# Optimization experiments

Measured on AMD Instinct MI355X. Metric: run time of the kernel, lower is better.

The kernel has to match this reference:

```python
import jax, jax.numpy as jnp
import numpy as np

EPSILON = 1e-06

def setup_inputs() -> dict:
    key = jax.random.key(0)
    k1, k2, k3 = jax.random.split(key, 3)
    B, S, D = 4, 4096, 4096
    x = jax.random.normal(k1, (B, S, D), dtype=jnp.float32)
    residual = jax.random.normal(k2, (B, S, D), dtype=jnp.float32)
    gamma = jax.random.uniform(k3, (D,), dtype=jnp.float32)
    return {"x": x, "residual": residual, "gamma": gamma}

def reference(x, residual, gamma):
    # Pass 1: residual add + RMSNorm (row-wise over last dim)
    x_added = x + residual
    rstd = jax.lax.rsqrt(jnp.mean(jnp.square(x_added), axis=-1, keepdims=True) + EPSILON)
    output = x_added * rstd * gamma  # [B, S, D]
    # Pass 2: global abs-max dynamic int8 quantization
    max_val = jnp.max(jnp.abs(output))
    scale = max_val / 127.0
    q = jnp.clip(jnp.round(output / scale), -128, 127).astype(jnp.int8)
    return q
```

## Files before the change

kernel.cpp:

```cpp
#include <hip/hip_runtime.h>
#include <hip/hip_fp16.h>

#define DD 4096
#define NROWS 16384
#define EPS 1e-6f


struct H4 { __half2 a, b; };

__global__ __launch_bounds__(256) void pass1(
    const float* __restrict__ x, const float* __restrict__ res,
    const float* __restrict__ gamma, H4* __restrict__ yg,
    float* __restrict__ rstd, float* __restrict__ rowmax) {
  const int row = blockIdx.x;
  const int t = threadIdx.x;
  const float4* x4 = (const float4*)(x + (size_t)row * DD);
  const float4* r4 = (const float4*)(res + (size_t)row * DD);
  const float4* g4 = (const float4*)gamma;
  H4* yrow = yg + (size_t)row * (DD / 4);

  float ss = 0.f, mx = 0.f;
#pragma unroll
  for (int i = 0; i < 4; ++i) {
    const int idx = t + i * 256;
    float4 xv = x4[idx], rv = r4[idx], gv = g4[idx];
    float y0 = xv.x + rv.x, y1 = xv.y + rv.y;
    float y2 = xv.z + rv.z, y3 = xv.w + rv.w;
    ss += y0 * y0 + y1 * y1 + y2 * y2 + y3 * y3;
    float p0 = y0 * gv.x, p1 = y1 * gv.y, p2 = y2 * gv.z, p3 = y3 * gv.w;
    mx = fmaxf(mx, fmaxf(fmaxf(fabsf(p0), fabsf(p1)),
                         fmaxf(fabsf(p2), fabsf(p3))));
    H4 h;
    h.a = __floats2half2_rn(p0, p1);
    h.b = __floats2half2_rn(p2, p3);
    yrow[idx] = h;
  }

#pragma unroll
  for (int off = 32; off > 0; off >>= 1) {
    ss += __shfl_down(ss, off, 64);
    mx = fmaxf(mx, __shfl_down(mx, off, 64));
  }
  __shared__ float s_ss[4], s_mx[4];
  const int wave = t >> 6, lane = t & 63;
  if (lane == 0) { s_ss[wave] = ss; s_mx[wave] = mx; }
  __syncthreads();
  if (t == 0) {
    float tss = s_ss[0] + s_ss[1] + s_ss[2] + s_ss[3];
    float tmx = fmaxf(fmaxf(s_mx[0], s_mx[1]), fmaxf(s_mx[2], s_mx[3]));
    float rs = rsqrtf(tss * (1.0f / DD) + EPS);
    rstd[row] = rs;
    rowmax[row] = tmx * rs;
  }
}

__global__ __launch_bounds__(1024) void reduce_gmax(
    const float* __restrict__ rowmax, float* __restrict__ gmax) {
  const int t = threadIdx.x;
  float m = 0.f;
#pragma unroll
  for (int i = 0; i < NROWS / 1024; ++i) m = fmaxf(m, rowmax[t + i * 1024]);
#pragma unroll
  for (int off = 32; off > 0; off >>= 1) m = fmaxf(m, __shfl_down(m, off, 64));
  __shared__ float s[16];
  if ((t & 63) == 0) s[t >> 6] = m;
  __syncthreads();
  if (t == 0) {
    float r = s[0];
#pragma unroll
    for (int i = 1; i < 16; ++i) r = fmaxf(r, s[i]);
    *gmax = r;
  }
}

__global__ __launch_bounds__(256) void pass2(
    const __half* __restrict__ yg, const float* __restrict__ rstd,
    const float* __restrict__ gmax, int* __restrict__ out) {
  const int row = blockIdx.x >> 1;
  const float c = rstd[row] * (127.0f / *gmax);
  const size_t base = ((size_t)blockIdx.x * 256 + threadIdx.x) * 8;
  union { int4 v; __half h[8]; } u;
  u.v = *(const int4*)(yg + base);
  int4 q0, q1;
  q0.x = min(max(__float2int_rn(__half2float(u.h[0]) * c), -128), 127);
  q0.y = min(max(__float2int_rn(__half2float(u.h[1]) * c), -128), 127);
  q0.z = min(max(__float2int_rn(__half2float(u.h[2]) * c), -128), 127);
  q0.w = min(max(__float2int_rn(__half2float(u.h[3]) * c), -128), 127);
  q1.x = min(max(__float2int_rn(__half2float(u.h[4]) * c), -128), 127);
  q1.y = min(max(__float2int_rn(__half2float(u.h[5]) * c), -128), 127);
  q1.z = min(max(__float2int_rn(__half2float(u.h[6]) * c), -128), 127);
  q1.w = min(max(__float2int_rn(__half2float(u.h[7]) * c), -128), 127);
  *(int4*)(out + base) = q0;
  *(int4*)(out + base + 4) = q1;
}

__global__ __launch_bounds__(256) void pass1_nb(
    const float* __restrict__ x, const float* __restrict__ res,
    const float* __restrict__ gamma, float* __restrict__ rstd,
    float* __restrict__ rowmax) {
  const int row = blockIdx.x;
  const int t = threadIdx.x;
  const float4* x4 = (const float4*)(x + (size_t)row * DD);
  const float4* r4 = (const float4*)(res + (size_t)row * DD);
  const float4* g4 = (const float4*)gamma;
  float ss = 0.f, mx = 0.f;
#pragma unroll
  for (int i = 0; i < 4; ++i) {
    const int idx = t + i * 256;
    float4 xv = x4[idx], rv = r4[idx], gv = g4[idx];
    float y0 = xv.x + rv.x, y1 = xv.y + rv.y;
    float y2 = xv.z + rv.z, y3 = xv.w + rv.w;
    ss += y0 * y0 + y1 * y1 + y2 * y2 + y3 * y3;
    mx = fmaxf(mx, fmaxf(fmaxf(fabsf(y0 * gv.x), fabsf(y1 * gv.y)),
                         fmaxf(fabsf(y2 * gv.z), fabsf(y3 * gv.w))));
  }
#pragma unroll
  for (int off = 32; off > 0; off >>= 1) {
    ss += __shfl_down(ss, off, 64);
    mx = fmaxf(mx, __shfl_down(mx, off, 64));
  }
  __shared__ float s_ss[4], s_mx[4];
  const int wave = t >> 6, lane = t & 63;
  if (lane == 0) { s_ss[wave] = ss; s_mx[wave] = mx; }
  __syncthreads();
  if (t == 0) {
    float tss = s_ss[0] + s_ss[1] + s_ss[2] + s_ss[3];
    float tmx = fmaxf(fmaxf(s_mx[0], s_mx[1]), fmaxf(s_mx[2], s_mx[3]));
    float rs = rsqrtf(tss * (1.0f / DD) + EPS);
    rstd[row] = rs;
    rowmax[row] = tmx * rs;
  }
}

__global__ __launch_bounds__(256) void pass2_nb(
    const float* __restrict__ x, const float* __restrict__ res,
    const float* __restrict__ gamma, const float* __restrict__ rstd,
    const float* __restrict__ gmax, int* __restrict__ out) {
  const int row = blockIdx.x;
  const int t = threadIdx.x;
  const float c = rstd[row] * (127.0f / *gmax);
  const float4* x4 = (const float4*)(x + (size_t)row * DD);
  const float4* r4 = (const float4*)(res + (size_t)row * DD);
  const float4* g4 = (const float4*)gamma;
  int4* o4 = (int4*)(out + (size_t)row * DD);
#pragma unroll
  for (int i = 0; i < 4; ++i) {
    const int idx = t + i * 256;
    float4 xv = x4[idx], rv = r4[idx], gv = g4[idx];
    int4 q;
    q.x = min(max(__float2int_rn((xv.x + rv.x) * gv.x * c), -128), 127);
    q.y = min(max(__float2int_rn((xv.y + rv.y) * gv.y * c), -128), 127);
    q.z = min(max(__float2int_rn((xv.z + rv.z) * gv.z * c), -128), 127);
    q.w = min(max(__float2int_rn((xv.w + rv.w) * gv.w * c), -128), 127);
    o4[idx] = q;
  }
}

extern "C" void kernel_launch(void* const* d_in, const int* in_sizes, int n_in,
                              void* d_out, int out_size, void* d_ws, size_t ws_size,
                              hipStream_t stream) {
  const float* x     = (const float*)d_in[0];
  const float* res   = (const float*)d_in[1];
  const float* gamma = (const float*)d_in[2];
  int* out = (int*)d_out;

  float* gmax   = (float*)d_ws;
  float* rowmax = (float*)((char*)d_ws + 256);
  float* rstd   = (float*)((char*)d_ws + 256 + NROWS * 4);
  const size_t yg_off = (size_t)1 << 20;
  const size_t need = yg_off + (size_t)NROWS * DD * 2;

  if (ws_size >= need) {
    H4* yg = (H4*)((char*)d_ws + yg_off);
    pass1<<<NROWS, 256, 0, stream>>>(x, res, gamma, yg, rstd, rowmax);
    reduce_gmax<<<1, 1024, 0, stream>>>(rowmax, gmax);
    pass2<<<((size_t)NROWS * DD) / 2048, 256, 0, stream>>>(
        (const __half*)yg, rstd, gmax, out);
  } else {
    pass1_nb<<<NROWS, 256, 0, stream>>>(x, res, gamma, rstd, rowmax);
    reduce_gmax<<<1, 1024, 0, stream>>>(rowmax, gmax);
    pass2_nb<<<NROWS, 256, 0, stream>>>(x, res, gamma, rstd, gmax, out);
  }
}
```

Baseline: 203.1 us.

## Map one wave per row in pass1 and use nontemporal loads/stores

Pass1 now assigns one 64-lane wave per row, four rows per block, so the block-level shared-memory reduction and __syncthreads are replaced by a pure wave shuffle reduction. The x and residual reads in pass1 and the int output writes in pass2 use nontemporal builtins, which are meant to reduce cache pollution from streaming data. Each lane now handles 16 float4 elements per row with partial unrolling, which raises per-thread work and may reduce the memory-level parallelism available per wave.

```diff
diff --git a/kernel.cpp b/kernel.cpp
--- a/kernel.cpp
+++ b/kernel.cpp
@@ -4,6 +4,9 @@
 #define DD 4096
 #define NROWS 16384
 #define EPS 1e-6f
+
+typedef float  fx4 __attribute__((ext_vector_type(4)));
+typedef int    ix4 __attribute__((ext_vector_type(4)));
 
 
 struct H4 { __half2 a, b; };
@@ -12,18 +15,22 @@
     const float* __restrict__ x, const float* __restrict__ res,
     const float* __restrict__ gamma, H4* __restrict__ yg,
     float* __restrict__ rstd, float* __restrict__ rowmax) {
-  const int row = blockIdx.x;
-  const int t = threadIdx.x;
-  const float4* x4 = (const float4*)(x + (size_t)row * DD);
-  const float4* r4 = (const float4*)(res + (size_t)row * DD);
-  const float4* g4 = (const float4*)gamma;
+  const int wave = threadIdx.x >> 6;
+  const int lane = threadIdx.x & 63;
+  const int row = blockIdx.x * 4 + wave;
+
+  const fx4* x4 = (const fx4*)(x + (size_t)row * DD);
+  const fx4* r4 = (const fx4*)(res + (size_t)row * DD);
+  const fx4* g4 = (const fx4*)gamma;
   H4* yrow = yg + (size_t)row * (DD / 4);
 
   float ss = 0.f, mx = 0.f;
-#pragma unroll
-  for (int i = 0; i < 4; ++i) {
-    const int idx = t + i * 256;
-    float4 xv = x4[idx], rv = r4[idx], gv = g4[idx];
+#pragma unroll 4
+  for (int i = 0; i < 16; ++i) {
+    const int idx = i * 64 + lane;
+    fx4 xv = __builtin_nontemporal_load(&x4[idx]);
+    fx4 rv = __builtin_nontemporal_load(&r4[idx]);
+    fx4 gv = g4[idx];
     float y0 = xv.x + rv.x, y1 = xv.y + rv.y;
     float y2 = xv.z + rv.z, y3 = xv.w + rv.w;
     ss += y0 * y0 + y1 * y1 + y2 * y2 + y3 * y3;
@@ -41,16 +48,10 @@
     ss += __shfl_down(ss, off, 64);
     mx = fmaxf(mx, __shfl_down(mx, off, 64));
   }
-  __shared__ float s_ss[4], s_mx[4];
-  const int wave = t >> 6, lane = t & 63;
-  if (lane == 0) { s_ss[wave] = ss; s_mx[wave] = mx; }
-  __syncthreads();
-  if (t == 0) {
-    float tss = s_ss[0] + s_ss[1] + s_ss[2] + s_ss[3];
-    float tmx = fmaxf(fmaxf(s_mx[0], s_mx[1]), fmaxf(s_mx[2], s_mx[3]));
-    float rs = rsqrtf(tss * (1.0f / DD) + EPS);
+  if (lane == 0) {
+    float rs = rsqrtf(ss * (1.0f / DD) + EPS);
     rstd[row] = rs;
-    rowmax[row] = tmx * rs;
+    rowmax[row] = mx * rs;
   }
 }
 
@@ -79,9 +80,9 @@
   const int row = blockIdx.x >> 1;
   const float c = rstd[row] * (127.0f / *gmax);
   const size_t base = ((size_t)blockIdx.x * 256 + threadIdx.x) * 8;
-  union { int4 v; __half h[8]; } u;
-  u.v = *(const int4*)(yg + base);
-  int4 q0, q1;
+  union { ix4 v; __half h[8]; } u;
+  u.v = *(const ix4*)(yg + base);
+  ix4 q0, q1;
   q0.x = min(max(__float2int_rn(__half2float(u.h[0]) * c), -128), 127);
   q0.y = min(max(__float2int_rn(__half2float(u.h[1]) * c), -128), 127);
   q0.z = min(max(__float2int_rn(__half2float(u.h[2]) * c), -128), 127);
@@ -90,24 +91,25 @@
   q1.y = min(max(__float2int_rn(__half2float(u.h[5]) * c), -128), 127);
   q1.z = min(max(__float2int_rn(__half2float(u.h[6]) * c), -128), 127);
   q1.w = min(max(__float2int_rn(__half2float(u.h[7]) * c), -128), 127);
-  *(int4*)(out + base) = q0;
-  *(int4*)(out + base + 4) = q1;
+  __builtin_nontemporal_store(q0, (ix4*)(out + base));
+  __builtin_nontemporal_store(q1, (ix4*)(out + base + 4));
 }
 
 __global__ __launch_bounds__(256) void pass1_nb(
     const float* __restrict__ x, const float* __restrict__ res,
     const float* __restrict__ gamma, float* __restrict__ rstd,
     float* __restrict__ rowmax) {
-  const int row = blockIdx.x;
-  const int t = threadIdx.x;
-  const float4* x4 = (const float4*)(x + (size_t)row * DD);
-  const float4* r4 = (const float4*)(res + (size_t)row * DD);
-  const float4* g4 = (const float4*)gamma;
+  const int wave = threadIdx.x >> 6;
+  const int lane = threadIdx.x & 63;
+  const int row = blockIdx.x * 4 + wave;
+  const fx4* x4 = (const fx4*)(x + (size_t)row * DD);
+  const fx4* r4 = (const fx4*)(res + (size_t)row * DD);
+  const fx4* g4 = (const fx4*)gamma;
   float ss = 0.f, mx = 0.f;
-#pragma unroll
-  for (int i = 0; i < 4; ++i) {
-    const int idx = t + i * 256;
-    float4 xv = x4[idx], rv = r4[idx], gv = g4[idx];
+#pragma unroll 4
+  for (int i = 0; i < 16; ++i) {
+    const int idx = i * 64 + lane;
+    fx4 xv = x4[idx], rv = r4[idx], gv = g4[idx];
     float y0 = xv.x + rv.x, y1 = xv.y + rv.y;
     float y2 = xv.z + rv.z, y3 = xv.w + rv.w;
     ss += y0 * y0 + y1 * y1 + y2 * y2 + y3 * y3;
@@ -119,16 +121,10 @@
     ss += __shfl_down(ss, off, 64);
     mx = fmaxf(mx, __shfl_down(mx, off, 64));
   }
-  __shared__ float s_ss[4], s_mx[4];
-  const int wave = t >> 6, lane = t & 63;
-  if (lane == 0) { s_ss[wave] = ss; s_mx[wave] = mx; }
-  __syncthreads();
-  if (t == 0) {
-    float tss = s_ss[0] + s_ss[1] + s_ss[2] + s_ss[3];
-    float tmx = fmaxf(fmaxf(s_mx[0], s_mx[1]), fmaxf(s_mx[2], s_mx[3]));
-    float rs = rsqrtf(tss * (1.0f / DD) + EPS);
+  if (lane == 0) {
+    float rs = rsqrtf(ss * (1.0f / DD) + EPS);
     rstd[row] = rs;
-    rowmax[row] = tmx * rs;
+    rowmax[row] = mx * rs;
   }
 }
 
@@ -139,15 +135,15 @@
   const int row = blockIdx.x;
   const int t = threadIdx.x;
   const float c = rstd[row] * (127.0f / *gmax);
-  const float4* x4 = (const float4*)(x + (size_t)row * DD);
-  const float4* r4 = (const float4*)(res + (size_t)row * DD);
-  const float4* g4 = (const float4*)gamma;
-  int4* o4 = (int4*)(out + (size_t)row * DD);
+  const fx4* x4 = (const fx4*)(x + (size_t)row * DD);
+  const fx4* r4 = (const fx4*)(res + (size_t)row * DD);
+  const fx4* g4 = (const fx4*)gamma;
+  ix4* o4 = (ix4*)(out + (size_t)row * DD);
 #pragma unroll
   for (int i = 0; i < 4; ++i) {
     const int idx = t + i * 256;
-    float4 xv = x4[idx], rv = r4[idx], gv = g4[idx];
-    int4 q;
+    fx4 xv = x4[idx], rv = r4[idx], gv = g4[idx];
+    ix4 q;
     q.x = min(max(__float2int_rn((xv.x + rv.x) * gv.x * c), -128), 127);
     q.y = min(max(__float2int_rn((xv.y + rv.y) * gv.y * c), -128), 127);
     q.z = min(max(__float2int_rn((xv.z + rv.z) * gv.z * c), -128), 127);
@@ -172,12 +168,12 @@
 
   if (ws_size >= need) {
     H4* yg = (H4*)((char*)d_ws + yg_off);
-    pass1<<<NROWS, 256, 0, stream>>>(x, res, gamma, yg, rstd, rowmax);
+    pass1<<<NROWS / 4, 256, 0, stream>>>(x, res, gamma, yg, rstd, rowmax);
     reduce_gmax<<<1, 1024, 0, stream>>>(rowmax, gmax);
     pass2<<<((size_t)NROWS * DD) / 2048, 256, 0, stream>>>(
         (const __half*)yg, rstd, gmax, out);
   } else {
-    pass1_nb<<<NROWS, 256, 0, stream>>>(x, res, gamma, rstd, rowmax);
+    pass1_nb<<<NROWS / 4, 256, 0, stream>>>(x, res, gamma, rstd, rowmax);
     reduce_gmax<<<1, 1024, 0, stream>>>(rowmax, gmax);
     pass2_nb<<<NROWS, 256, 0, stream>>>(x, res, gamma, rstd, gmax, out);
   }
```

New measurement: 213.3 us. +5.0%, slower.
